# Performance work log

Hardware: AMD Instinct MI355X
Metric: run time of the kernel (lower is better)

## Reference

```python
import jax, jax.numpy as jnp
import numpy as np

IN_FEATURES = 1024
OUT_FEATURES = 1024
GRID_SIZE = 5
SPLINE_ORDER = 3
GRID_RANGE = (-1.0, 1.0)


def make_grid():
    h = (GRID_RANGE[1] - GRID_RANGE[0]) / GRID_SIZE
    knots = jnp.arange(-SPLINE_ORDER, GRID_SIZE + SPLINE_ORDER + 1, dtype=jnp.float32) * h + GRID_RANGE[0]
    return jnp.broadcast_to(knots, (IN_FEATURES, knots.shape[0]))  # (in, 12)


def b_splines(x, knots, p):
    # x: (B, in); knots: (in, nk). Cox-de Boor recursion, degree p.
    xs = x[:, :, None]                                   # (B, in, 1)
    bases = ((xs >= knots[None, :, :-1]) & (xs < knots[None, :, 1:])).astype(x.dtype)
    for k in range(1, p + 1):
        den1 = knots[:, k:-1] - knots[:, :-(k + 1)]
        den1 = jnp.where(den1 == 0, jnp.float32(1e-8), den1)
        den2 = knots[:, k + 1:] - knots[:, 1:-k]
        den2 = jnp.where(den2 == 0, jnp.float32(1e-8), den2)
        term1 = (xs - knots[None, :, :-(k + 1)]) / den1[None] * bases[:, :, :-1]
        term2 = (knots[None, :, k + 1:] - xs) / den2[None] * bases[:, :, 1:]
        bases = term1 + term2
    return bases  # (B, in, grid_size + p)


def setup_inputs() -> dict:
    key = jax.random.key(0)
    k1, k2, k3, k4 = jax.random.split(key, 4)
    K = GRID_SIZE + SPLINE_ORDER
    x = jax.random.normal(k1, (4096, IN_FEATURES), dtype=jnp.float32)
    base_weight = jax.random.normal(k2, (OUT_FEATURES, IN_FEATURES), dtype=jnp.float32) * (1.0 / np.sqrt(IN_FEATURES))
    spline_weight = jax.random.normal(k3, (OUT_FEATURES, IN_FEATURES, K), dtype=jnp.float32) * 0.02
    spline_scaler = jax.random.normal(k4, (OUT_FEATURES, IN_FEATURES), dtype=jnp.float32) * (1.0 / np.sqrt(IN_FEATURES))
    grid = make_grid()
    return {"x": x, "base_weight": base_weight, "spline_weight": spline_weight,
            "spline_scaler": spline_scaler, "grid": grid}


def reference(x, base_weight, spline_weight, spline_scaler, grid):
    base_out = jax.nn.silu(x) @ base_weight.T                      # (B, out)
    bases = b_splines(x, grid, SPLINE_ORDER)                       # (B, in, K)
    scaled_sw = spline_weight * spline_scaler[:, :, None]          # (out, in, K)
    spline_out = jnp.einsum('bik,oik->bo', bases, scaled_sw)       # (B, out)
    return base_out + spline_out
```

## Files before the change

kernel.cpp:

```cpp
#include <hip/hip_runtime.h>
#include <hip/hip_bf16.h>
#include <cstdint>
#include <cstddef>

#define AS1 __attribute__((address_space(1)))
#define AS3 __attribute__((address_space(3)))

typedef __bf16 bf16;
typedef __bf16 bf16x8 __attribute__((ext_vector_type(8)));
typedef float f32x4 __attribute__((ext_vector_type(4)));

static constexpr int M_ROWS = 4096;
static constexpr int N_COLS = 1024;
static constexpr int IN_F   = 1024;
static constexpr int K2     = IN_F * 9;
static constexpr int BK     = 32;
static constexpr int KT_CNT = K2 / BK;

static constexpr int GBK = 64;
static constexpr int GKT = K2 / GBK;


__device__ __forceinline__ void bases8(float x, float w8[8]) {
  float mf = x * 2.5f + 5.5f;
  int   m  = (int)floorf(mf);
  float u  = mf - (float)m;
  float u2 = u * u, u3 = u2 * u;
  float omu = 1.0f - u;
  const float s = 1.0f / 6.0f;
  float p0 = u3 * s;
  float p1 = (-3.f*u3 + 3.f*u2 + 3.f*u + 1.f) * s;
  float p2 = (3.f*u3 - 6.f*u2 + 4.f) * s;
  float p3 = omu * omu * omu * s;
  bool in = (m >= 0) && (m < 11);
#pragma unroll
  for (int j = 0; j < 8; ++j) {
    float v = 0.0f;
    v = (j == m)     ? p0 : v;
    v = (j == m - 1) ? p1 : v;
    v = (j == m - 2) ? p2 : v;
    v = (j == m - 3) ? p3 : v;
    w8[j] = in ? v : 0.0f;
  }
}

__global__ void expand_a(const float* __restrict__ x, bf16* __restrict__ A,
                         int r0) {
  int gid = blockIdx.x * blockDim.x + threadIdx.x;
  int b = gid >> 10;
  int i = gid & 1023;
  float xv = x[(size_t)r0 * IN_F + (size_t)gid];

  A[(size_t)b * K2 + i] = (bf16)(xv / (1.0f + __expf(-xv)));

  float w8[8];
  bases8(xv, w8);
  bf16x8 outv;
#pragma unroll
  for (int j = 0; j < 8; ++j) outv[j] = (bf16)w8[j];
  *(bf16x8*)(A + (size_t)b * K2 + IN_F + (size_t)i * 8) = outv;
}

__global__ void make_bt(const float* __restrict__ bw, const float* __restrict__ sw,
                        const float* __restrict__ sc, bf16* __restrict__ BT) {
  int gid = blockIdx.x * blockDim.x + threadIdx.x;
  int o = gid >> 10;
  int i = gid & 1023;

  BT[(size_t)o * K2 + i] = (bf16)bw[gid];

  float scale = sc[gid];
  const float4* swp = (const float4*)(sw + (size_t)gid * 8);
  float4 a = swp[0], b4 = swp[1];
  float wv[8] = {a.x, a.y, a.z, a.w, b4.x, b4.y, b4.z, b4.w};
  bf16x8 r;
#pragma unroll
  for (int j = 0; j < 8; ++j) r[j] = (bf16)(wv[j] * scale);
  *(bf16x8*)(BT + (size_t)o * K2 + IN_F + (size_t)i * 8) = r;
}

__global__ __launch_bounds__(256, 1) void gemm_fused(
    const bf16* __restrict__ A, const bf16* __restrict__ BT,
    float* __restrict__ out, int r0) {
  __shared__ bf16 As[4][128 * GBK];
  __shared__ bf16 Bs[4][128 * GBK];

  const int tid  = threadIdx.x;
  const int lane = tid & 63;
  const int w    = tid >> 6;
  const int row0 = (blockIdx.x >> 3) * 128;
  const int col0 = (blockIdx.x & 7) * 128;

  const int srow = lane >> 3;
  const int sch  = ((lane & 7) ^ srow) * 8;

  const int r  = lane & 15;
  const int q  = lane >> 4;
  const int wm = (w >> 1) * 64;
  const int wn = (w & 1) * 64;
  const int kc0 = ((0 + q) ^ (r & 7)) * 8;
  const int kc1 = ((4 + q) ^ (r & 7)) * 8;

  const bf16* aB = A  + (size_t)row0 * K2;
  const bf16* bB = BT + (size_t)col0 * K2;

  f32x4 acc[4][4];
#pragma unroll
  for (int mt = 0; mt < 4; ++mt)
#pragma unroll
    for (int nt = 0; nt < 4; ++nt)
      acc[mt][nt] = f32x4{0.f, 0.f, 0.f, 0.f};

  auto stage = [&](int sbuf, int kt) {
#pragma unroll
    for (int t = 0; t < 4; ++t) {
      const int rg = w * 32 + t * 8;
      const bf16* ga = aB + (size_t)(rg + srow) * K2 + kt * GBK + sch;
      __builtin_amdgcn_global_load_lds((const AS1 void*)ga,
                                       (AS3 void*)&As[sbuf][rg * GBK], 16, 0, 0);
      const bf16* gb = bB + (size_t)(rg + srow) * K2 + kt * GBK + sch;
      __builtin_amdgcn_global_load_lds((const AS1 void*)gb,
                                       (AS3 void*)&Bs[sbuf][rg * GBK], 16, 0, 0);
    }
  };

  stage(0, 0);
  stage(1, 1);

  for (int kt = 0; kt < GKT; ++kt) {
    if (kt + 2 < GKT) {
      stage((kt + 2) & 3, kt + 2);
      asm volatile("s_waitcnt vmcnt(16)" ::: "memory");
    } else if (kt + 2 == GKT) {
      asm volatile("s_waitcnt vmcnt(8)" ::: "memory");
    } else {
      asm volatile("s_waitcnt vmcnt(0)" ::: "memory");
    }
    __builtin_amdgcn_s_barrier();
    __builtin_amdgcn_sched_barrier(0);

    const bf16* as = As[kt & 3];
    const bf16* bs = Bs[kt & 3];

#pragma unroll
    for (int kk = 0; kk < 2; ++kk) {
      const int kc = kk ? kc1 : kc0;
      bf16x8 af[4], bfr[4];
#pragma unroll
      for (int mt = 0; mt < 4; ++mt)
        af[mt] = *(const bf16x8*)&as[(wm + mt * 16 + r) * GBK + kc];
#pragma unroll
      for (int nt = 0; nt < 4; ++nt)
        bfr[nt] = *(const bf16x8*)&bs[(wn + nt * 16 + r) * GBK + kc];
#pragma unroll
      for (int mt = 0; mt < 4; ++mt)
#pragma unroll
        for (int nt = 0; nt < 4; ++nt)
          acc[mt][nt] = __builtin_amdgcn_mfma_f32_16x16x32_bf16(
              af[mt], bfr[nt], acc[mt][nt], 0, 0, 0);
    }
  }

#pragma unroll
  for (int mt = 0; mt < 4; ++mt)
#pragma unroll
    for (int nt = 0; nt < 4; ++nt)
#pragma unroll
      for (int k = 0; k < 4; ++k) {
        int row = r0 + row0 + wm + mt * 16 + q * 4 + k;
        int col = col0 + wn + nt * 16 + r;
        out[(size_t)row * N_COLS + col] = acc[mt][nt][k];
      }
}

__global__ __launch_bounds__(256) void kan_fused_fallback(
    const float* __restrict__ x, const float* __restrict__ bw,
    const float* __restrict__ sw, const float* __restrict__ sc,
    float* __restrict__ out) {
  __shared__ bf16 As[64 * BK];
  __shared__ bf16 Bs[128 * BK];
  const int tid  = threadIdx.x;
  const int lane = tid & 63;
  const int w    = tid >> 6;
  const int col0 = blockIdx.x * 128;
  const int row0 = blockIdx.y * 64;
  const int srow = tid >> 2, sq = tid & 3;
  const int r = lane & 15, q = lane >> 4, wn = w * 32;

  f32x4 acc[4][2];
#pragma unroll
  for (int mt = 0; mt < 4; ++mt)
#pragma unroll
    for (int nt = 0; nt < 2; ++nt) acc[mt][nt] = f32x4{0,0,0,0};

  for (int kt = 0; kt < KT_CNT; ++kt) {
    if (kt < 32) {
      const int cc = sq * 8;
      const float4* xp = (const float4*)(x + (size_t)(row0+srow)*IN_F + kt*BK + cc);
      float4 a = xp[0], b4 = xp[1];
      float xv[8] = {a.x,a.y,a.z,a.w,b4.x,b4.y,b4.z,b4.w};
      bf16x8 av;
#pragma unroll
      for (int j = 0; j < 8; ++j) av[j] = (bf16)(xv[j] / (1.0f + __expf(-xv[j])));
      *(bf16x8*)&As[srow * BK + cc] = av;
#pragma unroll
      for (int h = 0; h < 2; ++h) {
        const float4* bp = (const float4*)(bw + (size_t)(col0+h*64+srow)*IN_F + kt*BK + cc);
        float4 c0 = bp[0], c1 = bp[1];
        float bv[8] = {c0.x,c0.y,c0.z,c0.w,c1.x,c1.y,c1.z,c1.w};
        bf16x8 bb;
#pragma unroll
        for (int j = 0; j < 8; ++j) bb[j] = (bf16)bv[j];
        *(bf16x8*)&Bs[(h*64+srow)*BK + cc] = bb;
      }
    } else {
      const int i = (kt - 32) * 4 + sq;
      float xv = x[(size_t)(row0+srow)*IN_F + i];
      float w8[8]; bases8(xv, w8);
      bf16x8 av;
#pragma unroll
      for (int j = 0; j < 8; ++j) av[j] = (bf16)w8[j];
      *(bf16x8*)&As[srow * BK + sq * 8] = av;
#pragma unroll
      for (int h = 0; h < 2; ++h) {
        const int o = col0 + h*64 + srow;
        float s1 = sc[(size_t)o*IN_F + i];
        const float4* sp = (const float4*)(sw + ((size_t)o*IN_F + i)*8);
        float4 c0 = sp[0], c1 = sp[1];
        float wv[8] = {c0.x,c0.y,c0.z,c0.w,c1.x,c1.y,c1.z,c1.w};
        bf16x8 bb;
#pragma unroll
        for (int j = 0; j < 8; ++j) bb[j] = (bf16)(wv[j]*s1);
        *(bf16x8*)&Bs[(h*64+srow)*BK + sq*8] = bb;
      }
    }
    __syncthreads();
    bf16x8 af[4], bfr[2];
#pragma unroll
    for (int mt = 0; mt < 4; ++mt)
      af[mt] = *(const bf16x8*)&As[(mt*16+r)*BK + q*8];
#pragma unroll
    for (int nt = 0; nt < 2; ++nt)
      bfr[nt] = *(const bf16x8*)&Bs[(wn+nt*16+r)*BK + q*8];
#pragma unroll
    for (int mt = 0; mt < 4; ++mt)
#pragma unroll
      for (int nt = 0; nt < 2; ++nt)
        acc[mt][nt] = __builtin_amdgcn_mfma_f32_16x16x32_bf16(af[mt], bfr[nt], acc[mt][nt], 0,0,0);
    __syncthreads();
  }
#pragma unroll
  for (int mt = 0; mt < 4; ++mt)
#pragma unroll
    for (int nt = 0; nt < 2; ++nt)
#pragma unroll
      for (int k = 0; k < 4; ++k)
        out[(size_t)(row0+mt*16+q*4+k)*N_COLS + col0+wn+nt*16+r] = acc[mt][nt][k];
}

extern "C" void kernel_launch(void* const* d_in, const int* in_sizes, int n_in,
                              void* d_out, int out_size, void* d_ws, size_t ws_size,
                              hipStream_t stream) {
  const float* x    = (const float*)d_in[0];
  const float* bw   = (const float*)d_in[1];
  const float* sw   = (const float*)d_in[2];
  const float* sc   = (const float*)d_in[3];
  float* out = (float*)d_out;

  const size_t BT_BYTES  = (size_t)N_COLS * K2 * sizeof(bf16);
  const size_t ROW_BYTES = (size_t)K2 * sizeof(bf16);
  int SL = 0;
  for (int cand = 4096; cand >= 128; cand >>= 1)
    if (BT_BYTES + (size_t)cand * ROW_BYTES <= ws_size) { SL = cand; break; }

  if (SL) {
    bf16* BT    = (bf16*)d_ws;
    bf16* Aslab = BT + (size_t)N_COLS * K2;
    make_bt<<<(N_COLS * IN_F) / 256, 256, 0, stream>>>(bw, sw, sc, BT);
    for (int r0 = 0; r0 < M_ROWS; r0 += SL) {
      expand_a<<<(SL * IN_F) / 256, 256, 0, stream>>>(x, Aslab, r0);
      gemm_fused<<<(SL / 128) * (N_COLS / 128), 256, 0, stream>>>(Aslab, BT, out, r0);
    }
  } else {
    kan_fused_fallback<<<dim3(N_COLS / 128, M_ROWS / 64), 256, 0, stream>>>(
        x, bw, sw, sc, out);
  }
  (void)in_sizes; (void)n_in; (void)out_size;
}
```

Measured before the change: 237.6 us.

## Split-K GEMM into two halves with partial buffers and a reduce kernel

The fused GEMM now splits the K dimension into two segments, launching twice as many blocks that write partial results to two workspace buffers, followed by a vectorized reduce_add kernel. LDS buffering drops from four stages to two so two blocks can fit per CU, and block indexing switches to column-major tile order for reuse of B tiles. This targets low occupancy and too few blocks (256 tiles on a large CU count) at the cost of extra partial-output traffic and an additional kernel launch. The old slab path is kept as a fallback when the workspace is too small.

```diff
diff --git a/kernel.cpp b/kernel.cpp
--- a/kernel.cpp
+++ b/kernel.cpp
@@ -79,17 +79,25 @@
   *(bf16x8*)(BT + (size_t)o * K2 + IN_F + (size_t)i * 8) = r;
 }
 
-__global__ __launch_bounds__(256, 1) void gemm_fused(
+__global__ __launch_bounds__(256, 2) void gemm_fused(
     const bf16* __restrict__ A, const bf16* __restrict__ BT,
-    float* __restrict__ out, int r0) {
-  __shared__ bf16 As[4][128 * GBK];
-  __shared__ bf16 Bs[4][128 * GBK];
+    float* __restrict__ d0, float* __restrict__ d1,
+    int r0, int mt_cnt, int kt_seg) {
+  __shared__ bf16 As[2][128 * GBK];
+  __shared__ bf16 Bs[2][128 * GBK];
 
   const int tid  = threadIdx.x;
   const int lane = tid & 63;
   const int w    = tid >> 6;
-  const int row0 = (blockIdx.x >> 3) * 128;
-  const int col0 = (blockIdx.x & 7) * 128;
+
+  const int bps = mt_cnt * 8;
+  int b   = blockIdx.x;
+  const int seg = b / bps;
+  b -= seg * bps;
+  const int row0 = (b % mt_cnt) * 128;
+  const int col0 = (b / mt_cnt) * 128;
+  float* __restrict__ dst = seg ? d1 : d0;
+  const int kt0 = seg * kt_seg;
 
   const int srow = lane >> 3;
   const int sch  = ((lane & 7) ^ srow) * 8;
@@ -124,14 +132,11 @@
     }
   };
 
-  stage(0, 0);
-  stage(1, 1);
-
-  for (int kt = 0; kt < GKT; ++kt) {
-    if (kt + 2 < GKT) {
-      stage((kt + 2) & 3, kt + 2);
-      asm volatile("s_waitcnt vmcnt(16)" ::: "memory");
-    } else if (kt + 2 == GKT) {
+  stage(0, kt0);
+  int buf = 0;
+  for (int i = 0; i < kt_seg; ++i) {
+    if (i + 1 < kt_seg) {
+      stage(buf ^ 1, kt0 + i + 1);
       asm volatile("s_waitcnt vmcnt(8)" ::: "memory");
     } else {
       asm volatile("s_waitcnt vmcnt(0)" ::: "memory");
@@ -139,8 +144,8 @@
     __builtin_amdgcn_s_barrier();
     __builtin_amdgcn_sched_barrier(0);
 
-    const bf16* as = As[kt & 3];
-    const bf16* bs = Bs[kt & 3];
+    const bf16* as = As[buf];
+    const bf16* bs = Bs[buf];
 
 #pragma unroll
     for (int kk = 0; kk < 2; ++kk) {
@@ -159,6 +164,8 @@
           acc[mt][nt] = __builtin_amdgcn_mfma_f32_16x16x32_bf16(
               af[mt], bfr[nt], acc[mt][nt], 0, 0, 0);
     }
+    __builtin_amdgcn_s_barrier();
+    buf ^= 1;
   }
 
 #pragma unroll
@@ -169,8 +176,17 @@
       for (int k = 0; k < 4; ++k) {
         int row = r0 + row0 + wm + mt * 16 + q * 4 + k;
         int col = col0 + wn + nt * 16 + r;
-        out[(size_t)row * N_COLS + col] = acc[mt][nt][k];
+        dst[(size_t)row * N_COLS + col] = acc[mt][nt][k];
       }
+}
+
+__global__ void reduce_add(const float* __restrict__ p0,
+                           const float* __restrict__ p1,
+                           float* __restrict__ out) {
+  int i = blockIdx.x * blockDim.x + threadIdx.x;
+  f32x4 a = ((const f32x4*)p0)[i];
+  f32x4 b = ((const f32x4*)p1)[i];
+  ((f32x4*)out)[i] = a + b;
 }
 
 __global__ __launch_bounds__(256) void kan_fused_fallback(
@@ -269,21 +285,36 @@
 
   const size_t BT_BYTES  = (size_t)N_COLS * K2 * sizeof(bf16);
   const size_t ROW_BYTES = (size_t)K2 * sizeof(bf16);
-  int SL = 0;
-  for (int cand = 4096; cand >= 128; cand >>= 1)
-    if (BT_BYTES + (size_t)cand * ROW_BYTES <= ws_size) { SL = cand; break; }
-
-  if (SL) {
-    bf16* BT    = (bf16*)d_ws;
-    bf16* Aslab = BT + (size_t)N_COLS * K2;
+  const size_t A_BYTES   = (size_t)M_ROWS * ROW_BYTES;
+  const size_t OUT_BYTES = (size_t)M_ROWS * N_COLS * sizeof(float);
+
+  if (BT_BYTES + A_BYTES + 2 * OUT_BYTES <= ws_size) {
+    bf16*  BT    = (bf16*)d_ws;
+    bf16*  Aslab = BT + (size_t)N_COLS * K2;
+    float* P0    = (float*)((char*)d_ws + BT_BYTES + A_BYTES);
+    float* P1    = P0 + (size_t)M_ROWS * N_COLS;
     make_bt<<<(N_COLS * IN_F) / 256, 256, 0, stream>>>(bw, sw, sc, BT);
-    for (int r0 = 0; r0 < M_ROWS; r0 += SL) {
-      expand_a<<<(SL * IN_F) / 256, 256, 0, stream>>>(x, Aslab, r0);
-      gemm_fused<<<(SL / 128) * (N_COLS / 128), 256, 0, stream>>>(Aslab, BT, out, r0);
-    }
+    expand_a<<<(M_ROWS * IN_F) / 256, 256, 0, stream>>>(x, Aslab, 0);
+    gemm_fused<<<2 * (M_ROWS / 128) * (N_COLS / 128), 256, 0, stream>>>(
+        Aslab, BT, P0, P1, 0, M_ROWS / 128, GKT / 2);
+    reduce_add<<<(M_ROWS * N_COLS) / (4 * 256), 256, 0, stream>>>(P0, P1, out);
   } else {
-    kan_fused_fallback<<<dim3(N_COLS / 128, M_ROWS / 64), 256, 0, stream>>>(
-        x, bw, sw, sc, out);
+    int SL = 0;
+    for (int cand = 4096; cand >= 128; cand >>= 1)
+      if (BT_BYTES + (size_t)cand * ROW_BYTES <= ws_size) { SL = cand; break; }
+    if (SL) {
+      bf16* BT    = (bf16*)d_ws;
+      bf16* Aslab = BT + (size_t)N_COLS * K2;
+      make_bt<<<(N_COLS * IN_F) / 256, 256, 0, stream>>>(bw, sw, sc, BT);
+      for (int r0 = 0; r0 < M_ROWS; r0 += SL) {
+        expand_a<<<(SL * IN_F) / 256, 256, 0, stream>>>(x, Aslab, r0);
+        gemm_fused<<<(SL / 128) * (N_COLS / 128), 256, 0, stream>>>(
+            Aslab, BT, out, out, r0, SL / 128, GKT);
+      }
+    } else {
+      kan_fused_fallback<<<dim3(N_COLS / 128, M_ROWS / 64), 256, 0, stream>>>(
+          x, bw, sw, sc, out);
+    }
   }
   (void)in_sizes; (void)n_in; (void)out_size;
 }
```

New measurement: 204.4 us. 14.0% less time.
